# Optimization experiments

Hardware: AMD Instinct MI355X
Metric: run time of the kernel (lower is better)

Reference implementation:

```python
import jax, jax.numpy as jnp
import numpy as np

B, C, D = 16384, 512, 512
EXT = 2
H = C * EXT
TAU = 1.0          # temperature_train
STEP = 0.05        # langevin_step_size
NOISE = 0.1        # langevin_noise
STEPS = 32         # langevin_steps


def setup_inputs() -> dict:
    key = jax.random.key(0)
    ks = jax.random.split(key, 8)
    s_in = 1.0 / np.sqrt(D)
    s_h = 1.0 / np.sqrt(H)
    return {
        'x': jax.random.normal(ks[0], (B, D), jnp.float32),
        'vanilla_components': jnp.abs(jax.random.normal(ks[1], (C, D), jnp.float32) * 0.1),
        'e_sp': jax.random.normal(ks[2], (C * D,), jnp.float32) * 0.1,
        'W1e': jax.random.normal(ks[3], (D, H), jnp.float32) * s_in,
        'b1e': jnp.zeros((H,), jnp.float32),
        'W2e': jax.random.normal(ks[4], (H, C), jnp.float32) * s_h,
        'b2e': jnp.zeros((C,), jnp.float32),
        'W1r': jax.random.normal(ks[5], (D, H), jnp.float32) * s_in,
        'b1r': jnp.zeros((H,), jnp.float32),
        'W2r': jax.random.normal(ks[6], (H, C), jnp.float32) * s_h,
        'b2r': jnp.zeros((C,), jnp.float32),
    }


def _langevin_gate(e, key):
    """Langevin MCMC on latent u with quadratic energy E(u)=0.5||u||^2 + <e,u>.
    Returns selection probability sigmoid(-u/tau)."""
    def step(u, k):
        grad = u + e  # dE/du
        u = u - STEP * grad + NOISE * jax.random.normal(k, u.shape, u.dtype)
        return u, None
    u, _ = jax.lax.scan(step, jnp.zeros_like(e), jax.random.split(key, STEPS))
    return jax.nn.sigmoid(-u / TAU)


def reference(x, vanilla_components, e_sp, W1e, b1e, W2e, b2e, W1r, b1r, W2r, b2r):
    k1, k2 = jax.random.split(jax.random.key(42))
    # non-negative components
    comps = jnp.abs(vanilla_components)  # [C, D]
    # fixed energy-based sparsity mask over component entries
    p_sp = _langevin_gate(e_sp, k1).reshape(C, D)
    comps = comps * p_sp
    # dynamic per-sample component selection energies via MLP
    h = jax.nn.relu(x @ W1e + b1e)          # [B, H]
    e_dyn = h @ W2e + b2e                   # [B, C]
    gate = _langevin_gate(e_dyn, k2)        # [B, C] soft gates (train mode)
    hr = jax.nn.relu(x @ W1r + b1r)         # [B, H]
    conc = (hr @ W2r + b2r) * gate          # [B, C]
    # aggregate: (concentration * components).sum over components -> [B, D]
    return conc @ comps
```

## Files before the change

kernel.cpp:

```cpp
#include <hip/hip_runtime.h>
#include <hip/hip_bf16.h>
#include <stdint.h>

#define Bn 16384
#define Cn 512
#define Dn 512
#define Hn 1024

typedef __attribute__((ext_vector_type(8))) short bf16x8;
typedef __attribute__((ext_vector_type(4))) float f32x4;

__device__ __forceinline__ ushort f2bf(float f) {
  uint32_t u = __float_as_uint(f);
  return (ushort)((u + 0x7fffu + ((u >> 16) & 1u)) >> 16);
}

__device__ __forceinline__ uint32_t rotl32(uint32_t v, int s) {
  return (v << s) | (v >> (32 - s));
}

__device__ __forceinline__ void threefry2x32(uint32_t k0, uint32_t k1,
                                             uint32_t x0, uint32_t x1,
                                             uint32_t& o0, uint32_t& o1) {
  const uint32_t k2 = k0 ^ k1 ^ 0x1BD11BDAu;
  x0 += k0; x1 += k1;
#define TFR(r) { x0 += x1; x1 = rotl32(x1, (r)); x1 ^= x0; }
  TFR(13) TFR(15) TFR(26) TFR(6)   x0 += k1; x1 += k2 + 1u;
  TFR(17) TFR(29) TFR(16) TFR(24)  x0 += k2; x1 += k0 + 2u;
  TFR(13) TFR(15) TFR(26) TFR(6)   x0 += k0; x1 += k1 + 3u;
  TFR(17) TFR(29) TFR(16) TFR(24)  x0 += k1; x1 += k2 + 4u;
  TFR(13) TFR(15) TFR(26) TFR(6)   x0 += k2; x1 += k0 + 5u;
#undef TFR
  o0 = x0; o1 = x1;
}

__device__ __forceinline__ float bits_to_normal(uint32_t bits) {
  float f = __uint_as_float((bits >> 9) | 0x3f800000u) - 1.0f;
  float x = f * 2.0f - 0x1.fffffep-1f;
  float w = -__logf(1.0f - x * x);
  float p;
  if (w < 5.0f) {
    w -= 2.5f;
    p =            2.81022636e-08f;
    p = fmaf(p, w, 3.43273939e-07f);
    p = fmaf(p, w, -3.5233877e-06f);
    p = fmaf(p, w, -4.39150654e-06f);
    p = fmaf(p, w, 0.00021858087f);
    p = fmaf(p, w, -0.00125372503f);
    p = fmaf(p, w, -0.00417768164f);
    p = fmaf(p, w, 0.246640727f);
    p = fmaf(p, w, 1.50140941f);
  } else {
    w = sqrtf(w) - 3.0f;
    p =            -0.000200214257f;
    p = fmaf(p, w, 0.000100950558f);
    p = fmaf(p, w, 0.00134934322f);
    p = fmaf(p, w, -0.00367342844f);
    p = fmaf(p, w, 0.00573950773f);
    p = fmaf(p, w, -0.0076224613f);
    p = fmaf(p, w, 0.00943887047f);
    p = fmaf(p, w, 1.00167406f);
    p = fmaf(p, w, 2.83297682f);
  }
  return 0x1.6a09e6p+0f * (p * x);
}

__device__ __forceinline__ float langevin_gate(float e, const uint32_t* __restrict__ keys,
                                               uint32_t j) {
  float u = 0.0f;
#pragma unroll 1
  for (int t = 0; t < 32; ++t) {
    uint32_t o0, o1;
    threefry2x32(keys[2 * t], keys[2 * t + 1], 0u, j, o0, o1);
    float n = bits_to_normal(o0 ^ o1);
    u = (u - 0.05f * (u + e)) + 0.1f * n;
  }
  return 1.0f / (1.0f + __expf(u));
}

__global__ void k_setup_keys(uint32_t* __restrict__ keys) {
  if (threadIdx.x != 0 || blockIdx.x != 0) return;
  uint32_t k1w0, k1w1, k2w0, k2w1;
  threefry2x32(0u, 42u, 0u, 0u, k1w0, k1w1);
  threefry2x32(0u, 42u, 0u, 1u, k2w0, k2w1);
  for (uint32_t t = 0; t < 32; ++t) {
    uint32_t w0, w1;
    threefry2x32(k1w0, k1w1, 0u, t, w0, w1);
    keys[2 * t] = w0; keys[2 * t + 1] = w1;
    threefry2x32(k2w0, k2w1, 0u, t, w0, w1);
    keys[64 + 2 * t] = w0; keys[64 + 2 * t + 1] = w1;
  }
}

__global__ __launch_bounds__(256) void k_static_mask(
    const float* __restrict__ vc, const float* __restrict__ e_sp,
    const uint32_t* __restrict__ keys, ushort* __restrict__ compsT) {
  uint32_t j = blockIdx.x * 256 + threadIdx.x;
  uint32_t c = j & (Cn - 1), d = j >> 9;
  uint32_t ridx = c * Dn + d;
  float g = langevin_gate(e_sp[ridx], keys, ridx);
  compsT[j] = f2bf(fabsf(vc[ridx]) * g);
}

__global__ __launch_bounds__(256) void k_dyn_gate(
    float* __restrict__ eg, const uint32_t* __restrict__ keys) {
  uint32_t j = blockIdx.x * 256 + threadIdx.x;
  eg[j] = langevin_gate(eg[j], keys, j);
}

__global__ __launch_bounds__(256) void k_cvt_x(const float* __restrict__ in,
                                               ushort* __restrict__ out) {
  int i = (blockIdx.x * 256 + threadIdx.x) * 4;
  float4 v = *(const float4*)(in + i);
  ushort4 o = make_ushort4(f2bf(v.x), f2bf(v.y), f2bf(v.z), f2bf(v.w));
  *(ushort4*)(out + i) = o;
}

__global__ __launch_bounds__(256) void k_transpose_cvt(
    const float* __restrict__ in, ushort* __restrict__ out, int NO, int KO) {
  int o = blockIdx.x * 256 + threadIdx.x;
  int n = o / KO, k = o % KO;
  out[o] = f2bf(in[(size_t)k * NO + n]);
}

template <bool RELU, bool HASBIAS, bool GATEMUL, bool OUTBF16>
__global__ __launch_bounds__(256) void k_gemm_mfma(
    const ushort* __restrict__ A,
    const ushort* __restrict__ WT,
    const float* __restrict__ bias,
    const float* __restrict__ gate,
    void* __restrict__ Cout, int M, int N, int K) {
  __shared__ ushort As[128][40];
  __shared__ ushort Bs[128][40];

  const int t = threadIdx.x;
  const int m0 = blockIdx.y * 128, n0 = blockIdx.x * 128;

  const int srow = t >> 1;
  const int skoff = (t & 1) << 4;
  const ushort* Ap = A + (size_t)(m0 + srow) * K + skoff;
  const ushort* Bp = WT + (size_t)(n0 + srow) * K + skoff;

  const int wave = t >> 6, lane = t & 63;
  const int wm = (wave >> 1) << 6;
  const int wn = (wave & 1) << 6;
  const int quad = lane >> 4, l15 = lane & 15;

  f32x4 acc[4][4] = {};

  for (int k0 = 0; k0 < K; k0 += 32) {
    uint4 av0 = *(const uint4*)(Ap + k0);
    uint4 av1 = *(const uint4*)(Ap + k0 + 8);
    uint4 bv0 = *(const uint4*)(Bp + k0);
    uint4 bv1 = *(const uint4*)(Bp + k0 + 8);
    *(uint4*)&As[srow][skoff] = av0;
    *(uint4*)&As[srow][skoff + 8] = av1;
    *(uint4*)&Bs[srow][skoff] = bv0;
    *(uint4*)&Bs[srow][skoff + 8] = bv1;
    __syncthreads();

    bf16x8 af[4], bfr[4];
#pragma unroll
    for (int i = 0; i < 4; ++i) {
      af[i] = *(const bf16x8*)&As[wm + i * 16 + l15][quad * 8];
      bfr[i] = *(const bf16x8*)&Bs[wn + i * 16 + l15][quad * 8];
    }
#pragma unroll
    for (int i = 0; i < 4; ++i)
#pragma unroll
      for (int j = 0; j < 4; ++j)
        acc[i][j] = __builtin_amdgcn_mfma_f32_16x16x32_bf16(af[i], bfr[j],
                                                            acc[i][j], 0, 0, 0);
    __syncthreads();
  }

#pragma unroll
  for (int i = 0; i < 4; ++i) {
#pragma unroll
    for (int j = 0; j < 4; ++j) {
      const int col = n0 + wn + j * 16 + l15;
      float bv = HASBIAS ? bias[col] : 0.0f;
#pragma unroll
      for (int r = 0; r < 4; ++r) {
        const int row = m0 + wm + i * 16 + quad * 4 + r;
        float c = acc[i][j][r];
        if (HASBIAS) c += bv;
        if (RELU) c = fmaxf(c, 0.0f);
        if (GATEMUL) c *= gate[(size_t)row * N + col];
        if (OUTBF16)
          ((ushort*)Cout)[(size_t)row * N + col] = f2bf(c);
        else
          ((float*)Cout)[(size_t)row * N + col] = c;
      }
    }
  }
}

extern "C" void kernel_launch(void* const* d_in, const int* in_sizes, int n_in,
                              void* d_out, int out_size, void* d_ws, size_t ws_size,
                              hipStream_t stream) {
  const float* x    = (const float*)d_in[0];
  const float* vc   = (const float*)d_in[1];
  const float* e_sp = (const float*)d_in[2];
  const float* W1e  = (const float*)d_in[3];
  const float* b1e  = (const float*)d_in[4];
  const float* W2e  = (const float*)d_in[5];
  const float* b2e  = (const float*)d_in[6];
  const float* W1r  = (const float*)d_in[7];
  const float* b1r  = (const float*)d_in[8];
  const float* W2r  = (const float*)d_in[9];
  const float* b2r  = (const float*)d_in[10];
  float* out = (float*)d_out;

  char* ws = (char*)d_ws;
  uint32_t* keys = (uint32_t*)ws;
  ushort* W1eT   = (ushort*)(ws + (1u << 12));
  ushort* W2eT   = (ushort*)(ws + (1u << 12) + (1u << 20));
  ushort* W1rT   = (ushort*)(ws + (1u << 12) + (2u << 20));
  ushort* W2rT   = (ushort*)(ws + (1u << 12) + (3u << 20));
  ushort* compsT = (ushort*)(ws + (1u << 12) + (4u << 20));
  ushort* x_bf   = (ushort*)(ws + (8u << 20));
  ushort* conc   = x_bf;
  ushort* h_bf   = (ushort*)(ws + (24u << 20));
  float*  eg     = (float*)(ws + (56u << 20));

  k_setup_keys<<<1, 64, 0, stream>>>(keys);
  k_cvt_x<<<(Bn * Dn / 4) / 256, 256, 0, stream>>>(x, x_bf);
  k_transpose_cvt<<<(Dn * Hn) / 256, 256, 0, stream>>>(W1e, W1eT, Hn, Dn);
  k_transpose_cvt<<<(Hn * Cn) / 256, 256, 0, stream>>>(W2e, W2eT, Cn, Hn);
  k_transpose_cvt<<<(Dn * Hn) / 256, 256, 0, stream>>>(W1r, W1rT, Hn, Dn);
  k_transpose_cvt<<<(Hn * Cn) / 256, 256, 0, stream>>>(W2r, W2rT, Cn, Hn);
  k_static_mask<<<(Cn * Dn) / 256, 256, 0, stream>>>(vc, e_sp, keys, compsT);
  k_gemm_mfma<true, true, false, true><<<dim3(Hn / 128, Bn / 128), 256, 0, stream>>>(
      x_bf, W1eT, b1e, nullptr, h_bf, Bn, Hn, Dn);
  k_gemm_mfma<false, true, false, false><<<dim3(Cn / 128, Bn / 128), 256, 0, stream>>>(
      h_bf, W2eT, b2e, nullptr, eg, Bn, Cn, Hn);
  k_dyn_gate<<<(Bn * Cn) / 256, 256, 0, stream>>>(eg, keys + 64);
  k_gemm_mfma<true, true, false, true><<<dim3(Hn / 128, Bn / 128), 256, 0, stream>>>(
      x_bf, W1rT, b1r, nullptr, h_bf, Bn, Hn, Dn);
  k_gemm_mfma<false, true, true, true><<<dim3(Cn / 128, Bn / 128), 256, 0, stream>>>(
      h_bf, W2rT, b2r, eg, conc, Bn, Cn, Hn);
  k_gemm_mfma<false, false, false, false><<<dim3(Dn / 128, Bn / 128), 256, 0, stream>>>(
      conc, compsT, nullptr, nullptr, out, Bn, Dn, Cn);
}
```

Baseline: 891.5 us.

## Precompute Langevin noise sums and fuse gates, MLP GEMMs into a mega-kernel

Because the Langevin update is linear in u, the dynamic gate is rewritten in closed form: u_32 = -(1-0.95^32)*e + Z, where Z is the accumulated noise. Z depends only on the keys, so it is computed with no data dependence and shares one launch with the first-layer GEMMs and the static mask, which also fold the x fp32-to-bf16 conversion into their loads. The two second-layer GEMMs are fused into one kernel that applies the sigmoid gate in the epilogue, and the dynamic-gate pass and fp32 energy buffer are removed. In exchange, the noise uses a single-branch inverse-erf polynomial that clamps w at 5, Z is stored in bf16, and h and hr now occupy separate buffers.

```diff
diff --git a/kernel.cpp b/kernel.cpp
--- a/kernel.cpp
+++ b/kernel.cpp
@@ -7,6 +7,8 @@
 #define Dn 512
 #define Hn 1024
 
+#define A32 0.80628851f
+
 typedef __attribute__((ext_vector_type(8))) short bf16x8;
 typedef __attribute__((ext_vector_type(4))) float f32x4;
 
@@ -14,9 +16,12 @@
   uint32_t u = __float_as_uint(f);
   return (ushort)((u + 0x7fffu + ((u >> 16) & 1u)) >> 16);
 }
+__device__ __forceinline__ float b2f(ushort u) {
+  return __uint_as_float((uint32_t)u << 16);
+}
 
 __device__ __forceinline__ uint32_t rotl32(uint32_t v, int s) {
-  return (v << s) | (v >> (32 - s));
+  return __builtin_rotateleft32(v, (uint32_t)s);
 }
 
 __device__ __forceinline__ void threefry2x32(uint32_t k0, uint32_t k1,
@@ -65,17 +70,21 @@
   return 0x1.6a09e6p+0f * (p * x);
 }
 
-__device__ __forceinline__ float langevin_gate(float e, const uint32_t* __restrict__ keys,
-                                               uint32_t j) {
-  float u = 0.0f;
-#pragma unroll 1
-  for (int t = 0; t < 32; ++t) {
-    uint32_t o0, o1;
-    threefry2x32(keys[2 * t], keys[2 * t + 1], 0u, j, o0, o1);
-    float n = bits_to_normal(o0 ^ o1);
-    u = (u - 0.05f * (u + e)) + 0.1f * n;
-  }
-  return 1.0f / (1.0f + __expf(u));
+__device__ __forceinline__ float bits_to_px(uint32_t bits) {
+  float f = __uint_as_float((bits >> 9) | 0x3f800000u) - 1.0f;
+  float x = f * 2.0f - 0x1.fffffep-1f;
+  float w = -__logf(fmaf(-x, x, 1.0f));
+  w = fminf(w, 5.0f) - 2.5f;
+  float p =      2.81022636e-08f;
+  p = fmaf(p, w, 3.43273939e-07f);
+  p = fmaf(p, w, -3.5233877e-06f);
+  p = fmaf(p, w, -4.39150654e-06f);
+  p = fmaf(p, w, 0.00021858087f);
+  p = fmaf(p, w, -0.00125372503f);
+  p = fmaf(p, w, -0.00417768164f);
+  p = fmaf(p, w, 0.246640727f);
+  p = fmaf(p, w, 1.50140941f);
+  return p * x;
 }
 
 __global__ void k_setup_keys(uint32_t* __restrict__ keys) {
@@ -92,30 +101,6 @@
   }
 }
 
-__global__ __launch_bounds__(256) void k_static_mask(
-    const float* __restrict__ vc, const float* __restrict__ e_sp,
-    const uint32_t* __restrict__ keys, ushort* __restrict__ compsT) {
-  uint32_t j = blockIdx.x * 256 + threadIdx.x;
-  uint32_t c = j & (Cn - 1), d = j >> 9;
-  uint32_t ridx = c * Dn + d;
-  float g = langevin_gate(e_sp[ridx], keys, ridx);
-  compsT[j] = f2bf(fabsf(vc[ridx]) * g);
-}
-
-__global__ __launch_bounds__(256) void k_dyn_gate(
-    float* __restrict__ eg, const uint32_t* __restrict__ keys) {
-  uint32_t j = blockIdx.x * 256 + threadIdx.x;
-  eg[j] = langevin_gate(eg[j], keys, j);
-}
-
-__global__ __launch_bounds__(256) void k_cvt_x(const float* __restrict__ in,
-                                               ushort* __restrict__ out) {
-  int i = (blockIdx.x * 256 + threadIdx.x) * 4;
-  float4 v = *(const float4*)(in + i);
-  ushort4 o = make_ushort4(f2bf(v.x), f2bf(v.y), f2bf(v.z), f2bf(v.w));
-  *(ushort4*)(out + i) = o;
-}
-
 __global__ __launch_bounds__(256) void k_transpose_cvt(
     const float* __restrict__ in, ushort* __restrict__ out, int NO, int KO) {
   int o = blockIdx.x * 256 + threadIdx.x;
@@ -123,42 +108,35 @@
   out[o] = f2bf(in[(size_t)k * NO + n]);
 }
 
-template <bool RELU, bool HASBIAS, bool GATEMUL, bool OUTBF16>
-__global__ __launch_bounds__(256) void k_gemm_mfma(
-    const ushort* __restrict__ A,
-    const ushort* __restrict__ WT,
-    const float* __restrict__ bias,
-    const float* __restrict__ gate,
-    void* __restrict__ Cout, int M, int N, int K) {
-  __shared__ ushort As[128][40];
-  __shared__ ushort Bs[128][40];
-
+
+__device__ __forceinline__ void gemm_tile_xf32(
+    const float* __restrict__ A, const ushort* __restrict__ WT,
+    const float* __restrict__ bias, ushort* __restrict__ Out, int g,
+    ushort As[128][40], ushort Bs[128][40]) {
+  const int n0 = (g & 7) * 128, m0 = (g >> 3) * 128;
   const int t = threadIdx.x;
-  const int m0 = blockIdx.y * 128, n0 = blockIdx.x * 128;
-
-  const int srow = t >> 1;
-  const int skoff = (t & 1) << 4;
-  const ushort* Ap = A + (size_t)(m0 + srow) * K + skoff;
-  const ushort* Bp = WT + (size_t)(n0 + srow) * K + skoff;
-
+  const int srow = t >> 1, skb = (t & 1) << 4;
+  const float*  Ap = A  + (size_t)(m0 + srow) * Dn + skb;
+  const ushort* Bp = WT + (size_t)(n0 + srow) * Dn + skb;
   const int wave = t >> 6, lane = t & 63;
-  const int wm = (wave >> 1) << 6;
-  const int wn = (wave & 1) << 6;
+  const int wm = (wave >> 1) << 6, wn = (wave & 1) << 6;
   const int quad = lane >> 4, l15 = lane & 15;
 
   f32x4 acc[4][4] = {};
-
-  for (int k0 = 0; k0 < K; k0 += 32) {
-    uint4 av0 = *(const uint4*)(Ap + k0);
-    uint4 av1 = *(const uint4*)(Ap + k0 + 8);
-    uint4 bv0 = *(const uint4*)(Bp + k0);
-    uint4 bv1 = *(const uint4*)(Bp + k0 + 8);
-    *(uint4*)&As[srow][skoff] = av0;
-    *(uint4*)&As[srow][skoff + 8] = av1;
-    *(uint4*)&Bs[srow][skoff] = bv0;
-    *(uint4*)&Bs[srow][skoff + 8] = bv1;
-    __syncthreads();
-
+  for (int k0 = 0; k0 < Dn; k0 += 32) {
+    float4 a0 = *(const float4*)(Ap + k0);
+    float4 a1 = *(const float4*)(Ap + k0 + 4);
+    float4 a2 = *(const float4*)(Ap + k0 + 8);
+    float4 a3 = *(const float4*)(Ap + k0 + 12);
+    uint4 b0 = *(const uint4*)(Bp + k0);
+    uint4 b1 = *(const uint4*)(Bp + k0 + 8);
+    *(ushort4*)&As[srow][skb + 0]  = make_ushort4(f2bf(a0.x), f2bf(a0.y), f2bf(a0.z), f2bf(a0.w));
+    *(ushort4*)&As[srow][skb + 4]  = make_ushort4(f2bf(a1.x), f2bf(a1.y), f2bf(a1.z), f2bf(a1.w));
+    *(ushort4*)&As[srow][skb + 8]  = make_ushort4(f2bf(a2.x), f2bf(a2.y), f2bf(a2.z), f2bf(a2.w));
+    *(ushort4*)&As[srow][skb + 12] = make_ushort4(f2bf(a3.x), f2bf(a3.y), f2bf(a3.z), f2bf(a3.w));
+    *(uint4*)&Bs[srow][skb] = b0;
+    *(uint4*)&Bs[srow][skb + 8] = b1;
+    __syncthreads();
     bf16x8 af[4], bfr[4];
 #pragma unroll
     for (int i = 0; i < 4; ++i) {
@@ -173,27 +151,222 @@
                                                             acc[i][j], 0, 0, 0);
     __syncthreads();
   }
-
-#pragma unroll
-  for (int i = 0; i < 4; ++i) {
+#pragma unroll
+  for (int i = 0; i < 4; ++i)
 #pragma unroll
     for (int j = 0; j < 4; ++j) {
       const int col = n0 + wn + j * 16 + l15;
-      float bv = HASBIAS ? bias[col] : 0.0f;
+      const float bv = bias[col];
 #pragma unroll
       for (int r = 0; r < 4; ++r) {
         const int row = m0 + wm + i * 16 + quad * 4 + r;
-        float c = acc[i][j][r];
-        if (HASBIAS) c += bv;
-        if (RELU) c = fmaxf(c, 0.0f);
-        if (GATEMUL) c *= gate[(size_t)row * N + col];
-        if (OUTBF16)
-          ((ushort*)Cout)[(size_t)row * N + col] = f2bf(c);
-        else
-          ((float*)Cout)[(size_t)row * N + col] = c;
+        Out[(size_t)row * Hn + col] = f2bf(fmaxf(acc[i][j][r] + bv, 0.0f));
       }
     }
-  }
+}
+
+__device__ __forceinline__ void smask_block(
+    const float* __restrict__ vc, const float* __restrict__ e_sp,
+    const uint32_t* __restrict__ keys, ushort* __restrict__ compsT, int g) {
+  uint32_t j = (uint32_t)g * 256 + threadIdx.x;
+  uint32_t c = j & (Cn - 1), d = j >> 9;
+  uint32_t ridx = c * Dn + d;
+  float e = e_sp[ridx];
+  float u = 0.0f;
+#pragma unroll 1
+  for (int t = 0; t < 32; ++t) {
+    uint32_t o0, o1;
+    threefry2x32(keys[2 * t], keys[2 * t + 1], 0u, ridx, o0, o1);
+    float n = bits_to_normal(o0 ^ o1);
+    u = (u - 0.05f * (u + e)) + 0.1f * n;
+  }
+  float gt = 1.0f / (1.0f + __expf(u));
+  compsT[j] = f2bf(fabsf(vc[ridx]) * gt);
+}
+
+__device__ __forceinline__ void zdyn_block(
+    const uint32_t* __restrict__ keys, ushort* __restrict__ Z, uint32_t rb) {
+  const uint32_t j0 = (rb * 256u + threadIdx.x) * 4u;
+  float z0 = 0.0f, z1 = 0.0f, z2 = 0.0f, z3 = 0.0f;
+#pragma unroll 4
+  for (int t = 0; t < 32; ++t) {
+    const uint32_t K0 = keys[2 * t], K1 = keys[2 * t + 1];
+    uint32_t a0, b0, a1, b1, a2, b2, a3, b3;
+    threefry2x32(K0, K1, 0u, j0 + 0u, a0, b0);
+    threefry2x32(K0, K1, 0u, j0 + 1u, a1, b1);
+    threefry2x32(K0, K1, 0u, j0 + 2u, a2, b2);
+    threefry2x32(K0, K1, 0u, j0 + 3u, a3, b3);
+    z0 = fmaf(0.95f, z0, bits_to_px(a0 ^ b0) * 0.14142135f);
+    z1 = fmaf(0.95f, z1, bits_to_px(a1 ^ b1) * 0.14142135f);
+    z2 = fmaf(0.95f, z2, bits_to_px(a2 ^ b2) * 0.14142135f);
+    z3 = fmaf(0.95f, z3, bits_to_px(a3 ^ b3) * 0.14142135f);
+  }
+  *(ushort4*)(Z + j0) = make_ushort4(f2bf(z0), f2bf(z1), f2bf(z2), f2bf(z3));
+}
+
+__global__ __launch_bounds__(256) void k_mega(
+    const float* __restrict__ x,
+    const ushort* __restrict__ W1eT, const float* __restrict__ b1e, ushort* __restrict__ h,
+    const ushort* __restrict__ W1rT, const float* __restrict__ b1r, ushort* __restrict__ hr,
+    const float* __restrict__ vc, const float* __restrict__ e_sp,
+    const uint32_t* __restrict__ keys, ushort* __restrict__ compsT,
+    ushort* __restrict__ Zdyn) {
+  __shared__ ushort As[128][40];
+  __shared__ ushort Bs[128][40];
+  const uint32_t bx = blockIdx.x;
+  const uint32_t group = bx / 11u, pos = bx % 11u;
+  if (pos == 0u)
+    gemm_tile_xf32(x, W1eT, b1e, h, (int)group, As, Bs);
+  else if (pos == 1u)
+    gemm_tile_xf32(x, W1rT, b1r, hr, (int)group, As, Bs);
+  else if (pos == 2u)
+    smask_block(vc, e_sp, keys, compsT, (int)group);
+  else
+    zdyn_block(keys + 64, Zdyn, group * 8u + (pos - 3u));
+}
+
+__global__ __launch_bounds__(256) void k_dgemm(
+    const ushort* __restrict__ h, const ushort* __restrict__ W2eT,
+    const float* __restrict__ b2e,
+    const ushort* __restrict__ hr, const ushort* __restrict__ W2rT,
+    const float* __restrict__ b2r,
+    ushort* __restrict__ Zconc) {
+  __shared__ ushort As[128][40];
+  __shared__ ushort Bs[128][40];
+  const int t = threadIdx.x;
+  const int m0 = blockIdx.y * 128, n0 = blockIdx.x * 128;
+  const int srow = t >> 1, skb = (t & 1) << 4;
+  const int wave = t >> 6, lane = t & 63;
+  const int wm = (wave >> 1) << 6, wn = (wave & 1) << 6;
+  const int quad = lane >> 4, l15 = lane & 15;
+
+  const ushort* Ap = h    + (size_t)(m0 + srow) * Hn + skb;
+  const ushort* Bp = W2eT + (size_t)(n0 + srow) * Hn + skb;
+  f32x4 acc[4][4] = {};
+  for (int k0 = 0; k0 < Hn; k0 += 32) {
+    uint4 a0 = *(const uint4*)(Ap + k0);
+    uint4 a1 = *(const uint4*)(Ap + k0 + 8);
+    uint4 b0 = *(const uint4*)(Bp + k0);
+    uint4 b1 = *(const uint4*)(Bp + k0 + 8);
+    *(uint4*)&As[srow][skb] = a0; *(uint4*)&As[srow][skb + 8] = a1;
+    *(uint4*)&Bs[srow][skb] = b0; *(uint4*)&Bs[srow][skb + 8] = b1;
+    __syncthreads();
+    bf16x8 af[4], bfr[4];
+#pragma unroll
+    for (int i = 0; i < 4; ++i) {
+      af[i] = *(const bf16x8*)&As[wm + i * 16 + l15][quad * 8];
+      bfr[i] = *(const bf16x8*)&Bs[wn + i * 16 + l15][quad * 8];
+    }
+#pragma unroll
+    for (int i = 0; i < 4; ++i)
+#pragma unroll
+      for (int j = 0; j < 4; ++j)
+        acc[i][j] = __builtin_amdgcn_mfma_f32_16x16x32_bf16(af[i], bfr[j],
+                                                            acc[i][j], 0, 0, 0);
+    __syncthreads();
+  }
+  float g[4][4][4];
+#pragma unroll
+  for (int i = 0; i < 4; ++i)
+#pragma unroll
+    for (int j = 0; j < 4; ++j) {
+      const int col = n0 + wn + j * 16 + l15;
+      const float bv = b2e[col];
+#pragma unroll
+      for (int r = 0; r < 4; ++r) {
+        const int row = m0 + wm + i * 16 + quad * 4 + r;
+        float e = acc[i][j][r] + bv;
+        float z = b2f(Zconc[(size_t)row * Cn + col]);
+        g[i][j][r] = 1.0f / (1.0f + __expf(z - A32 * e));
+        acc[i][j][r] = 0.0f;
+      }
+    }
+  Ap = hr   + (size_t)(m0 + srow) * Hn + skb;
+  Bp = W2rT + (size_t)(n0 + srow) * Hn + skb;
+  for (int k0 = 0; k0 < Hn; k0 += 32) {
+    uint4 a0 = *(const uint4*)(Ap + k0);
+    uint4 a1 = *(const uint4*)(Ap + k0 + 8);
+    uint4 b0 = *(const uint4*)(Bp + k0);
+    uint4 b1 = *(const uint4*)(Bp + k0 + 8);
+    __syncthreads();
+    *(uint4*)&As[srow][skb] = a0; *(uint4*)&As[srow][skb + 8] = a1;
+    *(uint4*)&Bs[srow][skb] = b0; *(uint4*)&Bs[srow][skb + 8] = b1;
+    __syncthreads();
+    bf16x8 af[4], bfr[4];
+#pragma unroll
+    for (int i = 0; i < 4; ++i) {
+      af[i] = *(const bf16x8*)&As[wm + i * 16 + l15][quad * 8];
+      bfr[i] = *(const bf16x8*)&Bs[wn + i * 16 + l15][quad * 8];
+    }
+#pragma unroll
+    for (int i = 0; i < 4; ++i)
+#pragma unroll
+      for (int j = 0; j < 4; ++j)
+        acc[i][j] = __builtin_amdgcn_mfma_f32_16x16x32_bf16(af[i], bfr[j],
+                                                            acc[i][j], 0, 0, 0);
+  }
+#pragma unroll
+  for (int i = 0; i < 4; ++i)
+#pragma unroll
+    for (int j = 0; j < 4; ++j) {
+      const int col = n0 + wn + j * 16 + l15;
+      const float bv = b2r[col];
+#pragma unroll
+      for (int r = 0; r < 4; ++r) {
+        const int row = m0 + wm + i * 16 + quad * 4 + r;
+        Zconc[(size_t)row * Cn + col] = f2bf((acc[i][j][r] + bv) * g[i][j][r]);
+      }
+    }
+}
+
+__global__ __launch_bounds__(256) void k_gemm_out(
+    const ushort* __restrict__ A, const ushort* __restrict__ WT,
+    float* __restrict__ Out) {
+  __shared__ ushort As[128][40];
+  __shared__ ushort Bs[128][40];
+  const int t = threadIdx.x;
+  const int m0 = blockIdx.y * 128, n0 = blockIdx.x * 128;
+  const int srow = t >> 1, skb = (t & 1) << 4;
+  const ushort* Ap = A  + (size_t)(m0 + srow) * Cn + skb;
+  const ushort* Bp = WT + (size_t)(n0 + srow) * Cn + skb;
+  const int wave = t >> 6, lane = t & 63;
+  const int wm = (wave >> 1) << 6, wn = (wave & 1) << 6;
+  const int quad = lane >> 4, l15 = lane & 15;
+
+  f32x4 acc[4][4] = {};
+  for (int k0 = 0; k0 < Cn; k0 += 32) {
+    uint4 a0 = *(const uint4*)(Ap + k0);
+    uint4 a1 = *(const uint4*)(Ap + k0 + 8);
+    uint4 b0 = *(const uint4*)(Bp + k0);
+    uint4 b1 = *(const uint4*)(Bp + k0 + 8);
+    *(uint4*)&As[srow][skb] = a0; *(uint4*)&As[srow][skb + 8] = a1;
+    *(uint4*)&Bs[srow][skb] = b0; *(uint4*)&Bs[srow][skb + 8] = b1;
+    __syncthreads();
+    bf16x8 af[4], bfr[4];
+#pragma unroll
+    for (int i = 0; i < 4; ++i) {
+      af[i] = *(const bf16x8*)&As[wm + i * 16 + l15][quad * 8];
+      bfr[i] = *(const bf16x8*)&Bs[wn + i * 16 + l15][quad * 8];
+    }
+#pragma unroll
+    for (int i = 0; i < 4; ++i)
+#pragma unroll
+      for (int j = 0; j < 4; ++j)
+        acc[i][j] = __builtin_amdgcn_mfma_f32_16x16x32_bf16(af[i], bfr[j],
+                                                            acc[i][j], 0, 0, 0);
+    __syncthreads();
+  }
+#pragma unroll
+  for (int i = 0; i < 4; ++i)
+#pragma unroll
+    for (int j = 0; j < 4; ++j) {
+      const int col = n0 + wn + j * 16 + l15;
+#pragma unroll
+      for (int r = 0; r < 4; ++r) {
+        const int row = m0 + wm + i * 16 + quad * 4 + r;
+        Out[(size_t)row * Dn + col] = acc[i][j][r];
+      }
+    }
 }
 
 extern "C" void kernel_launch(void* const* d_in, const int* in_sizes, int n_in,
@@ -219,27 +392,18 @@
   ushort* W1rT   = (ushort*)(ws + (1u << 12) + (2u << 20));
   ushort* W2rT   = (ushort*)(ws + (1u << 12) + (3u << 20));
   ushort* compsT = (ushort*)(ws + (1u << 12) + (4u << 20));
-  ushort* x_bf   = (ushort*)(ws + (8u << 20));
-  ushort* conc   = x_bf;
+  ushort* Zdyn   = (ushort*)(ws + (8u << 20));
   ushort* h_bf   = (ushort*)(ws + (24u << 20));
-  float*  eg     = (float*)(ws + (56u << 20));
+  ushort* hr_bf  = (ushort*)(ws + (56u << 20));
 
   k_setup_keys<<<1, 64, 0, stream>>>(keys);
-  k_cvt_x<<<(Bn * Dn / 4) / 256, 256, 0, stream>>>(x, x_bf);
   k_transpose_cvt<<<(Dn * Hn) / 256, 256, 0, stream>>>(W1e, W1eT, Hn, Dn);
   k_transpose_cvt<<<(Hn * Cn) / 256, 256, 0, stream>>>(W2e, W2eT, Cn, Hn);
   k_transpose_cvt<<<(Dn * Hn) / 256, 256, 0, stream>>>(W1r, W1rT, Hn, Dn);
   k_transpose_cvt<<<(Hn * Cn) / 256, 256, 0, stream>>>(W2r, W2rT, Cn, Hn);
-  k_static_mask<<<(Cn * Dn) / 256, 256, 0, stream>>>(vc, e_sp, keys, compsT);
-  k_gemm_mfma<true, true, false, true><<<dim3(Hn / 128, Bn / 128), 256, 0, stream>>>(
-      x_bf, W1eT, b1e, nullptr, h_bf, Bn, Hn, Dn);
-  k_gemm_mfma<false, true, false, false><<<dim3(Cn / 128, Bn / 128), 256, 0, stream>>>(
-      h_bf, W2eT, b2e, nullptr, eg, Bn, Cn, Hn);
-  k_dyn_gate<<<(Bn * Cn) / 256, 256, 0, stream>>>(eg, keys + 64);
-  k_gemm_mfma<true, true, false, true><<<dim3(Hn / 128, Bn / 128), 256, 0, stream>>>(
-      x_bf, W1rT, b1r, nullptr, h_bf, Bn, Hn, Dn);
-  k_gemm_mfma<false, true, true, true><<<dim3(Cn / 128, Bn / 128), 256, 0, stream>>>(
-      h_bf, W2rT, b2r, eg, conc, Bn, Cn, Hn);
-  k_gemm_mfma<false, false, false, false><<<dim3(Dn / 128, Bn / 128), 256, 0, stream>>>(
-      conc, compsT, nullptr, nullptr, out, Bn, Dn, Cn);
-}
+  k_mega<<<11264, 256, 0, stream>>>(x, W1eT, b1e, h_bf, W1rT, b1r, hr_bf,
+                                    vc, e_sp, keys, compsT, Zdyn);
+  k_dgemm<<<dim3(Cn / 128, Bn / 128), 256, 0, stream>>>(
+      h_bf, W2eT, b2e, hr_bf, W2rT, b2r, Zdyn);
+  k_gemm_out<<<dim3(Dn / 128, Bn / 128), 256, 0, stream>>>(Zdyn, compsT, out);
+}
```

Measured after the change: 867.2 us. 1.03x faster.
